# Performance work log

Hardware: AMD Instinct MI355X
Metric: run time of the kernel (lower is better)

Reference implementation:

```python
import jax, jax.numpy as jnp
import numpy as np

D_MODEL = 2048
HEADS = 16


def setup_inputs() -> dict:
    key = jax.random.key(0)
    ks = jax.random.split(key, 9)
    s = 1.0 / np.sqrt(D_MODEL)
    x = jax.random.normal(ks[0], (2, 2048, D_MODEL), dtype=jnp.float32)
    wq = jax.random.uniform(ks[1], (D_MODEL, D_MODEL), jnp.float32, -s, s)
    wk = jax.random.uniform(ks[2], (D_MODEL, D_MODEL), jnp.float32, -s, s)
    wv = jax.random.uniform(ks[3], (D_MODEL, D_MODEL), jnp.float32, -s, s)
    wo = jax.random.uniform(ks[4], (D_MODEL, D_MODEL), jnp.float32, -s, s)
    bq = jax.random.uniform(ks[5], (D_MODEL,), jnp.float32, -s, s)
    bk = jax.random.uniform(ks[6], (D_MODEL,), jnp.float32, -s, s)
    bv = jax.random.uniform(ks[7], (D_MODEL,), jnp.float32, -s, s)
    bo = jax.random.uniform(ks[8], (D_MODEL,), jnp.float32, -s, s)
    return {"x": x, "wq": wq, "bq": bq, "wk": wk, "bk": bk,
            "wv": wv, "bv": bv, "wo": wo, "bo": bo}


def _split(t, heads):
    b, s, d = t.shape
    return t.reshape(b, s, heads, d // heads).transpose(0, 2, 1, 3)  # [b,h,s,dh]


def reference(x, wq, bq, wk, bk, wv, bv, wo, bo):
    q = x @ wq.T + bq
    k = x @ wk.T + bk
    v = x @ wv.T + bv
    q, k, v = _split(q, HEADS), _split(k, HEADS), _split(v, HEADS)
    dh = q.shape[-1]
    scale = 1.0 / np.sqrt(dh).astype(np.float32)
    score = jnp.einsum('bhqd,bhkd->bhqk', q, k) * scale  # [b,h,s,s]
    score = jax.nn.softmax(score.astype(jnp.float32), axis=-1).astype(q.dtype)
    out = jnp.einsum('bhqk,bhkd->bhqd', score, v)
    b, h, s, _ = out.shape
    out = out.transpose(0, 2, 1, 3).reshape(b, s, h * dh)
    return out @ wo.T + bo
```

## Files before the change

### kernel.cpp

```cpp
#include <hip/hip_runtime.h>
#include <cstdint>
#include <cstddef>

#define D_MODEL 2048
#define SEQ 2048
#define BATCH 2
#define HEADS 16
#define DH 128
#define MROWS (BATCH * SEQ)

typedef __attribute__((ext_vector_type(8))) short short8;
typedef __attribute__((ext_vector_type(4))) float f32x4;
typedef __attribute__((ext_vector_type(16))) float f32x16;
typedef __attribute__((ext_vector_type(2))) unsigned int uint2e;

__device__ __forceinline__ unsigned short f2bf(float f) {
    unsigned int u = __builtin_bit_cast(unsigned int, f);
    u += 0x7fffu + ((u >> 16) & 1u);
    return (unsigned short)(u >> 16);
}

__device__ __forceinline__ unsigned int cvt_pk_bf16(float lo, float hi) {
    unsigned int w;
    asm("v_cvt_pk_bf16_f32 %0, %1, %2" : "=v"(w) : "v"(lo), "v"(hi));
    return w;
}

__device__ __forceinline__ void swap32(unsigned int& x, unsigned int& y) {
#if __has_builtin(__builtin_amdgcn_permlane32_swap)
    uint2e r = __builtin_amdgcn_permlane32_swap(x, y, false, false);
    x = r[0]; y = r[1];
#else
    const int hi = (threadIdx.x >> 5) & 1;
    const unsigned int gx = (unsigned int)__shfl_xor((int)x, 32);
    const unsigned int gy = (unsigned int)__shfl_xor((int)y, 32);
    const unsigned int nx = hi ? gy : x;
    const unsigned int ny = hi ? y : gx;
    x = nx; y = ny;
#endif
}

__device__ __forceinline__ void gload_lds16(const unsigned short* g, unsigned short* l) {
    __builtin_amdgcn_global_load_lds(
        (const __attribute__((address_space(1))) void*)g,
        (__attribute__((address_space(3))) void*)l, 16, 0, 0);
}

__global__ __launch_bounds__(256) void cvt_kernel(const float* __restrict__ in,
                                                  unsigned short* __restrict__ out, int n4) {
    int i = blockIdx.x * 256 + threadIdx.x;
    if (i < n4) {
        const float4 v = reinterpret_cast<const float4*>(in)[i];
        ushort4 o;
        o.x = f2bf(v.x); o.y = f2bf(v.y); o.z = f2bf(v.z); o.w = f2bf(v.w);
        reinterpret_cast<ushort4*>(out)[i] = o;
    }
}

__global__ __launch_bounds__(256) void cvt4_kernel(const float* __restrict__ w0,
                                                   const float* __restrict__ w1,
                                                   const float* __restrict__ w2,
                                                   const float* __restrict__ w3,
                                                   unsigned short* __restrict__ out) {
    const int per = (D_MODEL * D_MODEL) / 4;
    int i = blockIdx.x * 256 + threadIdx.x;
    const int sel = i / per;
    const int off = i - sel * per;
    const float* s = sel == 0 ? w0 : sel == 1 ? w1 : sel == 2 ? w2 : w3;
    const float4 v = reinterpret_cast<const float4*>(s)[off];
    ushort4 o;
    o.x = f2bf(v.x); o.y = f2bf(v.y); o.z = f2bf(v.z); o.w = f2bf(v.w);
    reinterpret_cast<ushort4*>(out)[i] = o;
}

__global__ __launch_bounds__(512, 2)
void gemm8p(const unsigned short* __restrict__ A,
            const unsigned short* __restrict__ W0,
            const unsigned short* __restrict__ W1,
            const unsigned short* __restrict__ W2,
            const float* __restrict__ b0f,
            const float* __restrict__ b1f,
            const float* __restrict__ b2f,
            unsigned short* __restrict__ O0,
            unsigned short* __restrict__ O1,
            unsigned short* __restrict__ O2) {
    constexpr int BK = 64;
    constexpr int K = D_MODEL;
    constexpr int NT_N = 24;
    constexpr int NWG = 16 * NT_N;
    __shared__ unsigned short As[2][16384];
    __shared__ unsigned short Bs[2][16384];

    const int tid  = threadIdx.x;
    const int lane = tid & 63;
    const int wid  = tid >> 6;

    const int wk = (blockIdx.x & 7) * (NWG >> 3) + (blockIdx.x >> 3);
    const int nt = wk % NT_N;
    const int mt = wk / NT_N;
    const int m0 = mt * 256;
    const int nsel = nt >> 3;
    const int nloc = (nt & 7) * 256;

    const unsigned short* Bw = nsel == 0 ? W0 : (nsel == 1 ? W1 : W2);
    const float* bias = nsel == 0 ? b0f : (nsel == 1 ? b1f : b2f);

    const int srow = tid >> 3;
    const int sch  = tid & 7;
    const int ssw  = (sch ^ (srow & 7)) * 8;
    const int sd   = srow * 64 + sch * 8;
    const unsigned short* aS[4];
    const unsigned short* bS[4];
#pragma unroll
    for (int j = 0; j < 4; ++j) {
        aS[j] = A  + (size_t)(m0 + j * 64 + srow) * K + ssw;
        bS[j] = Bw + (size_t)(nloc + j * 64 + srow) * K + ssw;
    }

    const int fr = lane & 15, fg = lane >> 4;
    const int wm = wid >> 2, wn = wid & 3;
    int aoffs[2], boffs[2];
#pragma unroll
    for (int ks = 0; ks < 2; ++ks) {
        const int sw = ((ks * 4 + fg) ^ (fr & 7)) * 8;
        aoffs[ks] = (wm * 128 + fr) * 64 + sw;
        boffs[ks] = (wn * 64 + fr) * 64 + sw;
    }

    f32x4 acc[8][4] = {};

#define STG_F(SET, T)                                                \
    gload_lds16(aS[0] + (T) * BK, &As[SET][0 * 4096 + sd]);          \
    gload_lds16(aS[1] + (T) * BK, &As[SET][1 * 4096 + sd]);          \
    gload_lds16(bS[0] + (T) * BK, &Bs[SET][0 * 4096 + sd]);          \
    gload_lds16(bS[1] + (T) * BK, &Bs[SET][1 * 4096 + sd]);
#define STG_L(SET, T)                                                \
    gload_lds16(aS[2] + (T) * BK, &As[SET][2 * 4096 + sd]);          \
    gload_lds16(aS[3] + (T) * BK, &As[SET][3 * 4096 + sd]);          \
    gload_lds16(bS[2] + (T) * BK, &Bs[SET][2 * 4096 + sd]);          \
    gload_lds16(bS[3] + (T) * BK, &Bs[SET][3 * 4096 + sd]);
#define RD_A(DST, SET, HB)                                           \
    _Pragma("unroll") for (int mi = 0; mi < 4; ++mi)                 \
    _Pragma("unroll") for (int ks = 0; ks < 2; ++ks)                 \
        DST[mi][ks] = *(const short8*)&As[SET][(HB) + mi * 1024 + aoffs[ks]];
#define RD_B(DST, SET, NB)                                           \
    _Pragma("unroll") for (int ni = 0; ni < 2; ++ni)                 \
    _Pragma("unroll") for (int ks = 0; ks < 2; ++ks)                 \
        DST[ni][ks] = *(const short8*)&Bs[SET][((NB) + ni) * 1024 + boffs[ks]];
#define PH_MFMA(AF, BF, MB, NB)                                      \
    __builtin_amdgcn_s_barrier();                                    \
    asm volatile("s_waitcnt lgkmcnt(0)" ::: "memory");               \
    __builtin_amdgcn_sched_barrier(0);                               \
    __builtin_amdgcn_s_setprio(1);                                   \
    _Pragma("unroll") for (int ks = 0; ks < 2; ++ks)                 \
    _Pragma("unroll") for (int mi = 0; mi < 4; ++mi)                 \
    _Pragma("unroll") for (int ni = 0; ni < 2; ++ni)                 \
        acc[(MB) + mi][(NB) + ni] = __builtin_amdgcn_mfma_f32_16x16x32_bf16( \
            AF[mi][ks], BF[ni][ks], acc[(MB) + mi][(NB) + ni], 0, 0, 0);     \
    __builtin_amdgcn_s_setprio(0);                                   \
    __builtin_amdgcn_s_barrier();

    STG_F(0, 0)
    STG_L(0, 0)
    STG_F(1, 1)
    asm volatile("s_waitcnt vmcnt(4)" ::: "memory");
    __builtin_amdgcn_s_barrier();

#pragma unroll 1
    for (int j = 0; j < 16; ++j) {
        const int t0 = 2 * j;
        const bool more = (j < 15);
        short8 aF[4][2], aG[4][2], b01[2][2], b23[2][2];
        RD_A(aF, 0, 0)
        RD_B(b01, 0, 0)
        STG_L(1, t0 + 1)
        PH_MFMA(aF, b01, 0, 0)
        RD_B(b23, 0, 2)
        PH_MFMA(aF, b23, 0, 2)
        RD_A(aG, 0, 4096)
        PH_MFMA(aG, b23, 4, 2)
        if (more) {
            STG_F(0, t0 + 2)
            asm volatile("s_waitcnt vmcnt(4)" ::: "memory");
        } else {
            asm volatile("s_waitcnt vmcnt(0)" ::: "memory");
        }
        PH_MFMA(aG, b01, 4, 0)
        RD_A(aF, 1, 0)
        RD_B(b01, 1, 0)
        if (more) { STG_L(0, t0 + 2) }
        PH_MFMA(aF, b01, 0, 0)
        RD_B(b23, 1, 2)
        PH_MFMA(aF, b23, 0, 2)
        RD_A(aG, 1, 4096)
        PH_MFMA(aG, b23, 4, 2)
        if (more) {
            STG_F(1, t0 + 3)
            asm volatile("s_waitcnt vmcnt(4)" ::: "memory");
        }
        PH_MFMA(aG, b01, 4, 0)
    }
#undef STG_F
#undef STG_L
#undef RD_A
#undef RD_B
#undef PH_MFMA

    if (nsel == 2) {
#pragma unroll
        for (int mi = 0; mi < 8; ++mi)
#pragma unroll
            for (int ni = 0; ni < 4; ++ni) {
                const int col = nloc + wn * 64 + ni * 16 + fr;
                const int row0 = m0 + wm * 128 + mi * 16 + fg * 4;
                const float bv = bias[col];
                ushort4 o4;
                o4.x = f2bf(acc[mi][ni][0] + bv);
                o4.y = f2bf(acc[mi][ni][1] + bv);
                o4.z = f2bf(acc[mi][ni][2] + bv);
                o4.w = f2bf(acc[mi][ni][3] + bv);
                *(ushort4*)&O2[(size_t)col * MROWS + row0] = o4;
            }
    } else {
        unsigned short* Co = nsel ? O1 : O0;
#pragma unroll
        for (int mi = 0; mi < 8; ++mi)
#pragma unroll
            for (int ni = 0; ni < 4; ++ni) {
                const int col = nloc + wn * 64 + ni * 16 + fr;
                const float bv = bias[col];
#pragma unroll
                for (int r = 0; r < 4; ++r) {
                    const int row = m0 + wm * 128 + mi * 16 + fg * 4 + r;
                    Co[(size_t)row * D_MODEL + col] = f2bf(acc[mi][ni][r] + bv);
                }
            }
    }
}

template <int MODE>
__global__ __launch_bounds__(512, 2)
void gemmT(const unsigned short* __restrict__ A,
           const unsigned short* __restrict__ W0,
           const float* __restrict__ b0f,
           float* __restrict__ OF) {
    constexpr int BM = 256, BN = 128, BK = 64;
    constexpr int K = D_MODEL;
    constexpr int NTILES = K / BK;
    constexpr int NT_N = 16;
    constexpr int NWG = (MROWS / BM) * NT_N;
    __shared__ unsigned short As[3][BM * BK];
    __shared__ unsigned short Bs[3][BN * BK];

    const int tid  = threadIdx.x;
    const int lane = tid & 63;
    const int wid  = tid >> 6;

    const int wk = (blockIdx.x & 7) * (NWG >> 3) + (blockIdx.x >> 3);
    const int nt = wk % NT_N;
    const int mt = wk / NT_N;
    const int m0 = mt * BM;
    const int n0 = nt * BN;

    const unsigned short* Bw = W0;
    const float* bias = b0f;
    const int nloc = n0;

    const int srow = tid >> 3;
    const int sch  = tid & 7;
    const int ssw  = (sch ^ (srow & 7)) * 8;
    const int sd   = srow * 64 + sch * 8;
    const unsigned short* aS[4];
#pragma unroll
    for (int j = 0; j < 4; ++j) aS[j] = A + (size_t)(m0 + j * 64 + srow) * K + ssw;
    const unsigned short* bS[2];
#pragma unroll
    for (int j = 0; j < 2; ++j) bS[j] = Bw + (size_t)(nloc + j * 64 + srow) * K + ssw;

    const int fr = lane & 15, fg = lane >> 4;
    const int wm = wid >> 1, wn = wid & 1;
    int aoff[4][2], boff[4][2];
#pragma unroll
    for (int mi = 0; mi < 4; ++mi)
#pragma unroll
        for (int ks = 0; ks < 2; ++ks) {
            aoff[mi][ks] = (wm * 64 + mi * 16 + fr) * BK + ((ks * 4 + fg) ^ (fr & 7)) * 8;
            boff[mi][ks] = (wn * 64 + mi * 16 + fr) * BK + ((ks * 4 + fg) ^ (fr & 7)) * 8;
        }

    f32x4 acc[4][4] = {};

    unsigned short *pA0 = As[0], *pA1 = As[1], *pA2 = As[2];
    unsigned short *pB0 = Bs[0], *pB1 = Bs[1], *pB2 = Bs[2];

#define STG_A3(P, T) { _Pragma("unroll") for (int j = 0; j < 4; ++j) \
        gload_lds16(aS[j] + (T) * BK, (P) + j * 4096 + sd); }
#define STG_B3(P, T) { _Pragma("unroll") for (int j = 0; j < 2; ++j) \
        gload_lds16(bS[j] + (T) * BK, (P) + j * 4096 + sd); }

    STG_A3(pA0, 0) STG_B3(pB0, 0)
    STG_A3(pA1, 1) STG_B3(pB1, 1)
    asm volatile("s_waitcnt vmcnt(6)" ::: "memory");
    __builtin_amdgcn_s_barrier();

#pragma unroll 1
    for (int t = 0; t < NTILES; ++t) {
        const bool more = (t + 2 < NTILES);
        short8 aF[4][2], bF0[2][2];
#pragma unroll
        for (int mi = 0; mi < 4; ++mi)
#pragma unroll
            for (int ks = 0; ks < 2; ++ks)
                aF[mi][ks] = *(const short8*)&pA0[aoff[mi][ks]];
#pragma unroll
        for (int ni = 0; ni < 2; ++ni)
#pragma unroll
            for (int ks = 0; ks < 2; ++ks)
                bF0[ni][ks] = *(const short8*)&pB0[boff[ni][ks]];
        if (more) { STG_A3(pA2, t + 2) STG_B3(pB2, t + 2) }
        asm volatile("s_waitcnt lgkmcnt(0)" ::: "memory");
        __builtin_amdgcn_sched_barrier(0);
        __builtin_amdgcn_s_setprio(1);
#pragma unroll
        for (int ks = 0; ks < 2; ++ks)
#pragma unroll
            for (int mi = 0; mi < 4; ++mi)
#pragma unroll
                for (int ni = 0; ni < 2; ++ni)
                    acc[mi][ni] = __builtin_amdgcn_mfma_f32_16x16x32_bf16(
                        aF[mi][ks], bF0[ni][ks], acc[mi][ni], 0, 0, 0);
        __builtin_amdgcn_s_setprio(0);
        short8 bG[2][2];
#pragma unroll
        for (int ni = 0; ni < 2; ++ni)
#pragma unroll
            for (int ks = 0; ks < 2; ++ks)
                bG[ni][ks] = *(const short8*)&pB0[boff[2 + ni][ks]];
        asm volatile("s_waitcnt lgkmcnt(0)" ::: "memory");
        __builtin_amdgcn_sched_barrier(0);
        __builtin_amdgcn_s_setprio(1);
#pragma unroll
        for (int ks = 0; ks < 2; ++ks)
#pragma unroll
            for (int mi = 0; mi < 4; ++mi)
#pragma unroll
                for (int ni = 0; ni < 2; ++ni)
                    acc[mi][2 + ni] = __builtin_amdgcn_mfma_f32_16x16x32_bf16(
                        aF[mi][ks], bG[ni][ks], acc[mi][2 + ni], 0, 0, 0);
        __builtin_amdgcn_s_setprio(0);
        if (more) asm volatile("s_waitcnt vmcnt(6)" ::: "memory");
        else      asm volatile("s_waitcnt vmcnt(0)" ::: "memory");
        __builtin_amdgcn_s_barrier();
        unsigned short* tA = pA0; pA0 = pA1; pA1 = pA2; pA2 = tA;
        unsigned short* tB = pB0; pB0 = pB1; pB1 = pB2; pB2 = tB;
    }
#undef STG_A3
#undef STG_B3

#pragma unroll
    for (int mi = 0; mi < 4; ++mi)
#pragma unroll
        for (int ni = 0; ni < 4; ++ni) {
            const int col = nloc + wn * 64 + ni * 16 + fr;
            const float bv = bias[col];
#pragma unroll
            for (int r = 0; r < 4; ++r) {
                const int row = m0 + wm * 64 + mi * 16 + fg * 4 + r;
                OF[(size_t)row * D_MODEL + col] = acc[mi][ni][r] + bv;
            }
        }
}

__global__ __launch_bounds__(256, 2)
void flash_attn3(const unsigned short* __restrict__ Q, const unsigned short* __restrict__ Kg,
                 const unsigned short* __restrict__ VT, unsigned short* __restrict__ O) {
    constexpr int KVB = 64;
    constexpr int NT = SEQ / KVB;
    __shared__ unsigned short Ks[2 * KVB * DH];
    __shared__ unsigned short Vs[2 * DH * KVB];

    const int tid  = threadIdx.x;
    const int lane = tid & 63;
    const int wid  = tid >> 6;
    const int l31  = lane & 31;
    const int hi   = lane >> 5;

    const int qt = blockIdx.x & 15;
    const int bh = blockIdx.x >> 4;
    const int b = bh >> 4, h = bh & 15;
    const int qrow = qt * 128 + wid * 32 + l31;

    const unsigned short* Qp = Q + ((size_t)b * SEQ + qrow) * D_MODEL + h * DH;
    const unsigned short* Kp = Kg + (size_t)b * SEQ * D_MODEL + h * DH;
    const unsigned short* Vp = VT + (size_t)(h * DH) * MROWS + (size_t)b * SEQ;

    short8 qf[8];
#pragma unroll
    for (int kk = 0; kk < 8; ++kk)
        qf[kk] = *(const short8*)(Qp + kk * 16 + hi * 8);

    f32x16 acc[4] = {};
    float m_run = -1e30f, l_run = 0.f;
    const float Cc = 0.088388347648318447f * 1.4426950408889634f;
    const float THR = 8.0f / Cc;

    int co[8];
#pragma unroll
    for (int kk = 0; kk < 8; ++kk) co[kk] = ((kk * 2 + hi) ^ (l31 & 7)) * 8;

    int kroff[4], vroff[4];
#pragma unroll
    for (int q = 0; q < 4; ++q) {
        const int row_l = wid * 16 + q * 4 + (lane >> 4);
        kroff[q] = row_l * D_MODEL + ((lane & 15) ^ (row_l & 7)) * 8;
        const int d_l = wid * 32 + q * 8 + (lane >> 3);
        vroff[q] = d_l * MROWS + ((lane & 7) ^ (d_l & 7)) * 8;
    }
    unsigned short* KsW = Ks + (wid * 16) * DH;
    unsigned short* VsW = Vs + (wid * 32) * KVB;

#pragma unroll
    for (int q = 0; q < 4; ++q) {
        gload_lds16(Kp + kroff[q], KsW + q * 4 * DH);
        gload_lds16(Vp + vroff[q], VsW + q * 8 * KVB);
    }
    __syncthreads();

    for (int t = 0; t < NT; ++t) {
        const int cur = t & 1;
        if (t + 1 < NT) {
            const unsigned short* Kt = Kp + (size_t)((t + 1) * KVB) * D_MODEL;
            const unsigned short* Vt = Vp + (t + 1) * KVB;
            unsigned short* kd = KsW + (cur ^ 1) * (KVB * DH);
            unsigned short* vd = VsW + (cur ^ 1) * (DH * KVB);
#pragma unroll
            for (int q = 0; q < 4; ++q) {
                gload_lds16(Kt + kroff[q], kd + q * 4 * DH);
                gload_lds16(Vt + vroff[q], vd + q * 8 * KVB);
            }
        }
        const unsigned short* Kc = Ks + cur * (KVB * DH);
        const unsigned short* Vc = Vs + cur * (DH * KVB);

        f32x16 st0 = {}, st1 = {};
        __builtin_amdgcn_s_setprio(1);
#pragma unroll
        for (int kk = 0; kk < 8; ++kk) {
            const short8 kf0 = *(const short8*)&Kc[l31 * DH + co[kk]];
            const short8 kf1 = *(const short8*)&Kc[(32 + l31) * DH + co[kk]];
            st0 = __builtin_amdgcn_mfma_f32_32x32x16_bf16(kf0, qf[kk], st0, 0, 0, 0);
            st1 = __builtin_amdgcn_mfma_f32_32x32x16_bf16(kf1, qf[kk], st1, 0, 0, 0);
        }
        __builtin_amdgcn_s_setprio(0);

        float lm = -1e30f;
#pragma unroll
        for (int r = 0; r < 16; ++r) lm = fmaxf(lm, fmaxf(st0[r], st1[r]));
        {
            unsigned int a = __builtin_bit_cast(unsigned int, lm), bb = a;
            swap32(a, bb);
            lm = fmaxf(lm, __builtin_bit_cast(float, hi ? a : bb));
        }
        if (__any(lm > m_run + THR)) {
            const float mn = fmaxf(m_run, lm);
            const float sf = __builtin_amdgcn_exp2f((m_run - mn) * Cc);
            m_run = mn;
            l_run *= sf;
#pragma unroll
            for (int db = 0; db < 4; ++db)
#pragma unroll
                for (int r = 0; r < 16; ++r) acc[db][r] *= sf;
        }
        const float mc = m_run * Cc;
        float p0[16], p1[16];
        float ps = 0.f;
#pragma unroll
        for (int r = 0; r < 16; ++r) {
            p0[r] = __builtin_amdgcn_exp2f(__builtin_fmaf(st0[r], Cc, -mc));
            p1[r] = __builtin_amdgcn_exp2f(__builtin_fmaf(st1[r], Cc, -mc));
            ps += p0[r] + p1[r];
        }
        {
            unsigned int a = __builtin_bit_cast(unsigned int, ps), bb = a;
            swap32(a, bb);
            ps += __builtin_bit_cast(float, hi ? a : bb);
        }
        l_run += ps;

        unsigned int W0[8], W1[8];
#pragma unroll
        for (int tt = 0; tt < 8; ++tt) {
            W0[tt] = cvt_pk_bf16(p0[2 * tt], p0[2 * tt + 1]);
            W1[tt] = cvt_pk_bf16(p1[2 * tt], p1[2 * tt + 1]);
        }
        swap32(W0[0], W0[2]); swap32(W0[1], W0[3]);
        swap32(W0[4], W0[6]); swap32(W0[5], W0[7]);
        swap32(W1[0], W1[2]); swap32(W1[1], W1[3]);
        swap32(W1[4], W1[6]); swap32(W1[5], W1[7]);
        short8 pf[4];
        {
            uint4 f;
            f.x = W0[0]; f.y = W0[1]; f.z = W0[2]; f.w = W0[3];
            pf[0] = __builtin_bit_cast(short8, f);
            f.x = W0[4]; f.y = W0[5]; f.z = W0[6]; f.w = W0[7];
            pf[1] = __builtin_bit_cast(short8, f);
            f.x = W1[0]; f.y = W1[1]; f.z = W1[2]; f.w = W1[3];
            pf[2] = __builtin_bit_cast(short8, f);
            f.x = W1[4]; f.y = W1[5]; f.z = W1[6]; f.w = W1[7];
            pf[3] = __builtin_bit_cast(short8, f);
        }

        __builtin_amdgcn_s_setprio(1);
#pragma unroll
        for (int db = 0; db < 4; ++db) {
#pragma unroll
            for (int kk16 = 0; kk16 < 4; ++kk16) {
                const short8 vf = *(const short8*)&Vc[(db * 32 + l31) * KVB + co[kk16]];
                acc[db] = __builtin_amdgcn_mfma_f32_32x32x16_bf16(vf, pf[kk16], acc[db], 0, 0, 0);
            }
        }
        __builtin_amdgcn_s_setprio(0);
        __syncthreads();
    }

    const float inv_l = 1.0f / l_run;
    unsigned short* Op = O + ((size_t)b * SEQ + qrow) * D_MODEL + h * DH;
#pragma unroll
    for (int db = 0; db < 4; ++db)
#pragma unroll
        for (int g = 0; g < 4; ++g) {
            ushort4 o4;
            o4.x = f2bf(acc[db][4 * g + 0] * inv_l);
            o4.y = f2bf(acc[db][4 * g + 1] * inv_l);
            o4.z = f2bf(acc[db][4 * g + 2] * inv_l);
            o4.w = f2bf(acc[db][4 * g + 3] * inv_l);
            *(ushort4*)(Op + db * 32 + g * 8 + hi * 4) = o4;
        }
}

extern "C" void kernel_launch(void* const* d_in, const int* in_sizes, int n_in,
                              void* d_out, int out_size, void* d_ws, size_t ws_size,
                              hipStream_t stream) {
    (void)in_sizes; (void)n_in; (void)out_size; (void)ws_size;
    const float* x  = (const float*)d_in[0];
    const float* wq = (const float*)d_in[1];
    const float* bq = (const float*)d_in[2];
    const float* wk = (const float*)d_in[3];
    const float* bk = (const float*)d_in[4];
    const float* wv = (const float*)d_in[5];
    const float* bv = (const float*)d_in[6];
    const float* wo = (const float*)d_in[7];
    const float* bo = (const float*)d_in[8];
    float* out = (float*)d_out;

    unsigned short* ws = (unsigned short*)d_ws;
    const size_t NX = (size_t)MROWS * D_MODEL;
    const size_t NW = (size_t)D_MODEL * D_MODEL;
    unsigned short* xb  = ws;
    unsigned short* wqb = xb + NX;
    unsigned short* wkb = wqb + NW;
    unsigned short* wvb = wkb + NW;
    unsigned short* wob = wvb + NW;
    unsigned short* Qb  = wob + NW;
    unsigned short* Kb  = Qb + NX;
    unsigned short* VTb = Kb + NX;
    unsigned short* Ab  = VTb + NX;

    cvt_kernel<<<(unsigned)(NX / 1024), 256, 0, stream>>>(x, xb, (int)(NX / 4));
    cvt4_kernel<<<(unsigned)(4 * NW / 1024), 256, 0, stream>>>(wq, wk, wv, wo, wqb);

    gemm8p<<<384, 512, 0, stream>>>(xb, wqb, wkb, wvb, bq, bk, bv, Qb, Kb, VTb);

    flash_attn3<<<512, 256, 0, stream>>>(Qb, Kb, VTb, Ab);

    gemmT<1><<<256, 512, 0, stream>>>(Ab, wob, bo, out);
}
```

Before: 275.2 us.

## Split V projection into separate transposed GEMM for coalesced V^T stores

Removes the V projection from the fused QKV kernel, which now handles only Q and K on 256 workgroups. V^T is computed by a new kernel as Wv·X^T, so its output rows are contiguous along the sequence and the strided column-major scatter stores go away. The cost is one extra kernel launch and two grids of 256 workgroups instead of one grid of 384, which may change wave balance across CUs.

Result: faster. 250.5 us (-8.9%).

```diff
diff --git a/kernel.cpp b/kernel.cpp
--- a/kernel.cpp
+++ b/kernel.cpp
@@ -74,19 +74,16 @@
 }
 
 __global__ __launch_bounds__(512, 2)
-void gemm8p(const unsigned short* __restrict__ A,
-            const unsigned short* __restrict__ W0,
-            const unsigned short* __restrict__ W1,
-            const unsigned short* __restrict__ W2,
-            const float* __restrict__ b0f,
-            const float* __restrict__ b1f,
-            const float* __restrict__ b2f,
-            unsigned short* __restrict__ O0,
-            unsigned short* __restrict__ O1,
-            unsigned short* __restrict__ O2) {
+void gemm8qk(const unsigned short* __restrict__ A,
+             const unsigned short* __restrict__ W0,
+             const unsigned short* __restrict__ W1,
+             const float* __restrict__ b0f,
+             const float* __restrict__ b1f,
+             unsigned short* __restrict__ O0,
+             unsigned short* __restrict__ O1) {
     constexpr int BK = 64;
     constexpr int K = D_MODEL;
-    constexpr int NT_N = 24;
+    constexpr int NT_N = 16;
     constexpr int NWG = 16 * NT_N;
     __shared__ unsigned short As[2][16384];
     __shared__ unsigned short Bs[2][16384];
@@ -102,8 +99,8 @@
     const int nsel = nt >> 3;
     const int nloc = (nt & 7) * 256;
 
-    const unsigned short* Bw = nsel == 0 ? W0 : (nsel == 1 ? W1 : W2);
-    const float* bias = nsel == 0 ? b0f : (nsel == 1 ? b1f : b2f);
+    const unsigned short* Bw = nsel ? W1 : W0;
+    const float* bias = nsel ? b1f : b0f;
 
     const int srow = tid >> 3;
     const int sch  = tid & 7;
@@ -206,86 +203,64 @@
 #undef RD_B
 #undef PH_MFMA
 
-    if (nsel == 2) {
-#pragma unroll
-        for (int mi = 0; mi < 8; ++mi)
-#pragma unroll
-            for (int ni = 0; ni < 4; ++ni) {
-                const int col = nloc + wn * 64 + ni * 16 + fr;
-                const int row0 = m0 + wm * 128 + mi * 16 + fg * 4;
-                const float bv = bias[col];
-                ushort4 o4;
-                o4.x = f2bf(acc[mi][ni][0] + bv);
-                o4.y = f2bf(acc[mi][ni][1] + bv);
-                o4.z = f2bf(acc[mi][ni][2] + bv);
-                o4.w = f2bf(acc[mi][ni][3] + bv);
-                *(ushort4*)&O2[(size_t)col * MROWS + row0] = o4;
+    unsigned short* Co = nsel ? O1 : O0;
+#pragma unroll
+    for (int mi = 0; mi < 8; ++mi)
+#pragma unroll
+        for (int ni = 0; ni < 4; ++ni) {
+            const int col = nloc + wn * 64 + ni * 16 + fr;
+            const float bv = bias[col];
+#pragma unroll
+            for (int r = 0; r < 4; ++r) {
+                const int row = m0 + wm * 128 + mi * 16 + fg * 4 + r;
+                Co[(size_t)row * D_MODEL + col] = f2bf(acc[mi][ni][r] + bv);
             }
-    } else {
-        unsigned short* Co = nsel ? O1 : O0;
-#pragma unroll
-        for (int mi = 0; mi < 8; ++mi)
-#pragma unroll
-            for (int ni = 0; ni < 4; ++ni) {
-                const int col = nloc + wn * 64 + ni * 16 + fr;
-                const float bv = bias[col];
-#pragma unroll
-                for (int r = 0; r < 4; ++r) {
-                    const int row = m0 + wm * 128 + mi * 16 + fg * 4 + r;
-                    Co[(size_t)row * D_MODEL + col] = f2bf(acc[mi][ni][r] + bv);
-                }
-            }
-    }
-}
-
-template <int MODE>
+        }
+}
+
 __global__ __launch_bounds__(512, 2)
-void gemmT(const unsigned short* __restrict__ A,
-           const unsigned short* __restrict__ W0,
-           const float* __restrict__ b0f,
-           float* __restrict__ OF) {
-    constexpr int BM = 256, BN = 128, BK = 64;
+void gemmV(const unsigned short* __restrict__ Wv,
+           const unsigned short* __restrict__ X,
+           const float* __restrict__ bvf,
+           unsigned short* __restrict__ VT) {
+    constexpr int BK = 64;
     constexpr int K = D_MODEL;
     constexpr int NTILES = K / BK;
-    constexpr int NT_N = 16;
-    constexpr int NWG = (MROWS / BM) * NT_N;
-    __shared__ unsigned short As[3][BM * BK];
-    __shared__ unsigned short Bs[3][BN * BK];
+    constexpr int NWG = 256;
+    __shared__ unsigned short As[3][128 * BK];
+    __shared__ unsigned short Bs[3][256 * BK];
 
     const int tid  = threadIdx.x;
     const int lane = tid & 63;
     const int wid  = tid >> 6;
 
     const int wk = (blockIdx.x & 7) * (NWG >> 3) + (blockIdx.x >> 3);
-    const int nt = wk % NT_N;
-    const int mt = wk / NT_N;
-    const int m0 = mt * BM;
-    const int n0 = nt * BN;
-
-    const unsigned short* Bw = W0;
-    const float* bias = b0f;
-    const int nloc = n0;
+    const int nt = wk & 15;
+    const int mt = wk >> 4;
+    const int m0 = mt * 128;
+    const int n0 = nt * 256;
 
     const int srow = tid >> 3;
     const int sch  = tid & 7;
     const int ssw  = (sch ^ (srow & 7)) * 8;
     const int sd   = srow * 64 + sch * 8;
-    const unsigned short* aS[4];
-#pragma unroll
-    for (int j = 0; j < 4; ++j) aS[j] = A + (size_t)(m0 + j * 64 + srow) * K + ssw;
-    const unsigned short* bS[2];
-#pragma unroll
-    for (int j = 0; j < 2; ++j) bS[j] = Bw + (size_t)(nloc + j * 64 + srow) * K + ssw;
+    const unsigned short* aS[2];
+#pragma unroll
+    for (int j = 0; j < 2; ++j) aS[j] = Wv + (size_t)(m0 + j * 64 + srow) * K + ssw;
+    const unsigned short* bS[4];
+#pragma unroll
+    for (int j = 0; j < 4; ++j) bS[j] = X + (size_t)(n0 + j * 64 + srow) * K + ssw;
 
     const int fr = lane & 15, fg = lane >> 4;
-    const int wm = wid >> 1, wn = wid & 1;
+    const int wm = wid >> 2, wn = wid & 3;
     int aoff[4][2], boff[4][2];
 #pragma unroll
-    for (int mi = 0; mi < 4; ++mi)
+    for (int i = 0; i < 4; ++i)
 #pragma unroll
         for (int ks = 0; ks < 2; ++ks) {
-            aoff[mi][ks] = (wm * 64 + mi * 16 + fr) * BK + ((ks * 4 + fg) ^ (fr & 7)) * 8;
-            boff[mi][ks] = (wn * 64 + mi * 16 + fr) * BK + ((ks * 4 + fg) ^ (fr & 7)) * 8;
+            const int sw = ((ks * 4 + fg) ^ (fr & 7)) * 8;
+            aoff[i][ks] = (wm * 64 + i * 16 + fr) * BK + sw;
+            boff[i][ks] = (wn * 64 + i * 16 + fr) * BK + sw;
         }
 
     f32x4 acc[4][4] = {};
@@ -293,13 +268,13 @@
     unsigned short *pA0 = As[0], *pA1 = As[1], *pA2 = As[2];
     unsigned short *pB0 = Bs[0], *pB1 = Bs[1], *pB2 = Bs[2];
 
-#define STG_A3(P, T) { _Pragma("unroll") for (int j = 0; j < 4; ++j) \
+#define STG_AV(P, T) { _Pragma("unroll") for (int j = 0; j < 2; ++j) \
         gload_lds16(aS[j] + (T) * BK, (P) + j * 4096 + sd); }
-#define STG_B3(P, T) { _Pragma("unroll") for (int j = 0; j < 2; ++j) \
+#define STG_BV(P, T) { _Pragma("unroll") for (int j = 0; j < 4; ++j) \
         gload_lds16(bS[j] + (T) * BK, (P) + j * 4096 + sd); }
 
-    STG_A3(pA0, 0) STG_B3(pB0, 0)
-    STG_A3(pA1, 1) STG_B3(pB1, 1)
+    STG_AV(pA0, 0) STG_BV(pB0, 0)
+    STG_AV(pA1, 1) STG_BV(pB1, 1)
     asm volatile("s_waitcnt vmcnt(6)" ::: "memory");
     __builtin_amdgcn_s_barrier();
 
@@ -317,7 +292,7 @@
 #pragma unroll
             for (int ks = 0; ks < 2; ++ks)
                 bF0[ni][ks] = *(const short8*)&pB0[boff[ni][ks]];
-        if (more) { STG_A3(pA2, t + 2) STG_B3(pB2, t + 2) }
+        if (more) { STG_AV(pA2, t + 2) STG_BV(pB2, t + 2) }
         asm volatile("s_waitcnt lgkmcnt(0)" ::: "memory");
         __builtin_amdgcn_sched_barrier(0);
         __builtin_amdgcn_s_setprio(1);
@@ -354,6 +329,134 @@
         unsigned short* tA = pA0; pA0 = pA1; pA1 = pA2; pA2 = tA;
         unsigned short* tB = pB0; pB0 = pB1; pB1 = pB2; pB2 = tB;
     }
+#undef STG_AV
+#undef STG_BV
+
+#pragma unroll
+    for (int mi = 0; mi < 4; ++mi)
+#pragma unroll
+        for (int r = 0; r < 4; ++r) {
+            const int row = m0 + wm * 64 + mi * 16 + fg * 4 + r;
+            const float bv = bvf[row];
+#pragma unroll
+            for (int ni = 0; ni < 4; ++ni) {
+                const int col = n0 + wn * 64 + ni * 16 + fr;
+                VT[(size_t)row * MROWS + col] = f2bf(acc[mi][ni][r] + bv);
+            }
+        }
+}
+
+__global__ __launch_bounds__(512, 2)
+void gemmT1(const unsigned short* __restrict__ A,
+            const unsigned short* __restrict__ W0,
+            const float* __restrict__ b0f,
+            float* __restrict__ OF) {
+    constexpr int BM = 256, BN = 128, BK = 64;
+    constexpr int K = D_MODEL;
+    constexpr int NTILES = K / BK;
+    constexpr int NT_N = 16;
+    constexpr int NWG = (MROWS / BM) * NT_N;
+    __shared__ unsigned short As[3][BM * BK];
+    __shared__ unsigned short Bs[3][BN * BK];
+
+    const int tid  = threadIdx.x;
+    const int lane = tid & 63;
+    const int wid  = tid >> 6;
+
+    const int wk = (blockIdx.x & 7) * (NWG >> 3) + (blockIdx.x >> 3);
+    const int nt = wk % NT_N;
+    const int mt = wk / NT_N;
+    const int m0 = mt * BM;
+    const int n0 = nt * BN;
+
+    const int srow = tid >> 3;
+    const int sch  = tid & 7;
+    const int ssw  = (sch ^ (srow & 7)) * 8;
+    const int sd   = srow * 64 + sch * 8;
+    const unsigned short* aS[4];
+#pragma unroll
+    for (int j = 0; j < 4; ++j) aS[j] = A + (size_t)(m0 + j * 64 + srow) * K + ssw;
+    const unsigned short* bS[2];
+#pragma unroll
+    for (int j = 0; j < 2; ++j) bS[j] = W0 + (size_t)(n0 + j * 64 + srow) * K + ssw;
+
+    const int fr = lane & 15, fg = lane >> 4;
+    const int wm = wid >> 1, wn = wid & 1;
+    int aoff[4][2], boff[4][2];
+#pragma unroll
+    for (int mi = 0; mi < 4; ++mi)
+#pragma unroll
+        for (int ks = 0; ks < 2; ++ks) {
+            aoff[mi][ks] = (wm * 64 + mi * 16 + fr) * BK + ((ks * 4 + fg) ^ (fr & 7)) * 8;
+            boff[mi][ks] = (wn * 64 + mi * 16 + fr) * BK + ((ks * 4 + fg) ^ (fr & 7)) * 8;
+        }
+
+    f32x4 acc[4][4] = {};
+
+    unsigned short *pA0 = As[0], *pA1 = As[1], *pA2 = As[2];
+    unsigned short *pB0 = Bs[0], *pB1 = Bs[1], *pB2 = Bs[2];
+
+#define STG_A3(P, T) { _Pragma("unroll") for (int j = 0; j < 4; ++j) \
+        gload_lds16(aS[j] + (T) * BK, (P) + j * 4096 + sd); }
+#define STG_B3(P, T) { _Pragma("unroll") for (int j = 0; j < 2; ++j) \
+        gload_lds16(bS[j] + (T) * BK, (P) + j * 4096 + sd); }
+
+    STG_A3(pA0, 0) STG_B3(pB0, 0)
+    STG_A3(pA1, 1) STG_B3(pB1, 1)
+    asm volatile("s_waitcnt vmcnt(6)" ::: "memory");
+    __builtin_amdgcn_s_barrier();
+
+#pragma unroll 1
+    for (int t = 0; t < NTILES; ++t) {
+        const bool more = (t + 2 < NTILES);
+        short8 aF[4][2], bF0[2][2];
+#pragma unroll
+        for (int mi = 0; mi < 4; ++mi)
+#pragma unroll
+            for (int ks = 0; ks < 2; ++ks)
+                aF[mi][ks] = *(const short8*)&pA0[aoff[mi][ks]];
+#pragma unroll
+        for (int ni = 0; ni < 2; ++ni)
+#pragma unroll
+            for (int ks = 0; ks < 2; ++ks)
+                bF0[ni][ks] = *(const short8*)&pB0[boff[ni][ks]];
+        if (more) { STG_A3(pA2, t + 2) STG_B3(pB2, t + 2) }
+        asm volatile("s_waitcnt lgkmcnt(0)" ::: "memory");
+        __builtin_amdgcn_sched_barrier(0);
+        __builtin_amdgcn_s_setprio(1);
+#pragma unroll
+        for (int ks = 0; ks < 2; ++ks)
+#pragma unroll
+            for (int mi = 0; mi < 4; ++mi)
+#pragma unroll
+                for (int ni = 0; ni < 2; ++ni)
+                    acc[mi][ni] = __builtin_amdgcn_mfma_f32_16x16x32_bf16(
+                        aF[mi][ks], bF0[ni][ks], acc[mi][ni], 0, 0, 0);
+        __builtin_amdgcn_s_setprio(0);
+        short8 bG[2][2];
+#pragma unroll
+        for (int ni = 0; ni < 2; ++ni)
+#pragma unroll
+            for (int ks = 0; ks < 2; ++ks)
+                bG[ni][ks] = *(const short8*)&pB0[boff[2 + ni][ks]];
+        asm volatile("s_waitcnt lgkmcnt(0)" ::: "memory");
+        __builtin_amdgcn_sched_barrier(0);
+        __builtin_amdgcn_s_setprio(1);
+#pragma unroll
+        for (int ks = 0; ks < 2; ++ks)
+#pragma unroll
+            for (int mi = 0; mi < 4; ++mi)
+#pragma unroll
+                for (int ni = 0; ni < 2; ++ni)
+                    acc[mi][2 + ni] = __builtin_amdgcn_mfma_f32_16x16x32_bf16(
+                        aF[mi][ks], bG[ni][ks], acc[mi][2 + ni], 0, 0, 0);
+        __builtin_amdgcn_s_setprio(0);
+        if (more) asm volatile("s_waitcnt vmcnt(6)" ::: "memory");
+        else      asm volatile("s_waitcnt vmcnt(0)" ::: "memory");
+        __builtin_amdgcn_s_barrier();
+        unsigned short* tA = pA0; pA0 = pA1; pA1 = pA2; pA2 = tA;
+        unsigned short* tB = pB0; pB0 = pB1; pB1 = pB2; pB2 = tB;
+    }
 #undef STG_A3
 #undef STG_B3
 
@@ -361,8 +464,8 @@
     for (int mi = 0; mi < 4; ++mi)
 #pragma unroll
         for (int ni = 0; ni < 4; ++ni) {
-            const int col = nloc + wn * 64 + ni * 16 + fr;
-            const float bv = bias[col];
+            const int col = n0 + wn * 64 + ni * 16 + fr;
+            const float bv = b0f[col];
 #pragma unroll
             for (int r = 0; r < 4; ++r) {
                 const int row = m0 + wm * 64 + mi * 16 + fg * 4 + r;
@@ -569,9 +672,10 @@
     cvt_kernel<<<(unsigned)(NX / 1024), 256, 0, stream>>>(x, xb, (int)(NX / 4));
     cvt4_kernel<<<(unsigned)(4 * NW / 1024), 256, 0, stream>>>(wq, wk, wv, wo, wqb);
 
-    gemm8p<<<384, 512, 0, stream>>>(xb, wqb, wkb, wvb, bq, bk, bv, Qb, Kb, VTb);
+    gemm8qk<<<256, 512, 0, stream>>>(xb, wqb, wkb, bq, bk, Qb, Kb);
+    gemmV<<<256, 512, 0, stream>>>(wvb, xb, bv, VTb);
 
     flash_attn3<<<512, 256, 0, stream>>>(Qb, Kb, VTb, Ab);
 
-    gemmT<1><<<256, 512, 0, stream>>>(Ab, wob, bo, out);
-}
+    gemmT1<<<256, 512, 0, stream>>>(Ab, wob, bo, out);
+}
```
